# Optimization experiments

Hardware: AMD Instinct MI355X
Metric: run time of the kernel (lower is better)

Reference implementation:

```python
import jax, jax.numpy as jnp
import numpy as np

E = 16          # n_routed_experts
Z = 8           # zero_expert_num
K = 4           # moe_topk
H = 1024        # hidden_size
I = 768         # moe_intermediate_size
T = 2048        # tokens
SCALE = 2.5     # routed_scaling_factor


def setup_inputs() -> dict:
    key = jax.random.key(0)
    ks = jax.random.split(key, 6)
    return {
        "hidden_states": jax.random.normal(ks[0], (T, H), dtype=jnp.float32),
        "num_global_tokens": T,
        "max_num_tokens_per_gpu": T,
        "w_router": jax.random.normal(ks[1], (E + Z, H), dtype=jnp.float32) * 0.02,
        "correction_bias": jnp.zeros((E + Z,), dtype=jnp.float32),
        "wg": jax.random.normal(ks[2], (E, I, H), dtype=jnp.float32) * 0.02,
        "wu": jax.random.normal(ks[3], (E, I, H), dtype=jnp.float32) * 0.02,
        "wd": jax.random.normal(ks[4], (E, H, I), dtype=jnp.float32) * 0.02,
    }


def reference(hidden_states, num_global_tokens, max_num_tokens_per_gpu,
              w_router, correction_bias, wg, wu, wd):
    x = hidden_states
    # ---- router gemm (always fp32) ----
    logits = x.astype(jnp.float32) @ w_router.T                      # [T, E+Z]
    # ---- DeepSeekV3-style top-k: sigmoid scores, bias only for selection ----
    scores = jax.nn.sigmoid(logits)
    _, topk_ids = jax.lax.top_k(scores + correction_bias[None, :], K)  # [T, K]
    w = jnp.take_along_axis(scores, topk_ids, axis=-1)               # [T, K]
    w = w / jnp.sum(w, axis=-1, keepdims=True)                       # renormalize
    w = w * SCALE                                                    # routed_scaling_factor
    # ---- zero-expert masking (identity type) ----
    zero_mask = topk_ids >= E                                        # [T, K]
    zero_w = jnp.sum(jnp.where(zero_mask, w, 0.0), axis=-1, keepdims=True)
    ids = jnp.where(zero_mask, 0, topk_ids)
    w = jnp.where(zero_mask, 0.0, w)
    # ---- combine weights per (token, expert); masked slots add 0.0 ----
    cw = jnp.zeros((x.shape[0], E), dtype=jnp.float32)
    cw = cw.at[jnp.arange(x.shape[0])[:, None], ids].add(w)          # [T, E]
    # ---- grouped silu-gated expert MLPs (dense compute + masked combine) ----
    g = jnp.einsum('th,eih->eti', x, wg)                             # [E, T, I]
    u = jnp.einsum('th,eih->eti', x, wu)
    a = jax.nn.silu(g) * u
    y = jnp.einsum('eti,ehi->eth', a, wd)                            # [E, T, H]
    routed = jnp.einsum('eth,te->th', y, cw)                         # [T, H]
    return routed + x * zero_w.astype(x.dtype)
```

## Files before the change

kernel.cpp:

```cpp
#include <hip/hip_runtime.h>
#include <hip/hip_bf16.h>
#include <math.h>

typedef __bf16 bf16x8 __attribute__((ext_vector_type(8)));
typedef float f32x4 __attribute__((ext_vector_type(4)));

#define T_TOK 2048
#define HD 1024
#define ID 768
#define NE 16
#define NEZ 24
#define NK 4
#define SCALE_F 2.5f

#define MFMA(a, b, c) __builtin_amdgcn_mfma_f32_16x16x32_bf16(a, b, c, 0, 0, 0)

__device__ __forceinline__ unsigned short f2bf(float f) {
  unsigned int u = __builtin_bit_cast(unsigned int, f);
  u += 0x7FFFu + ((u >> 16) & 1u);
  return (unsigned short)(u >> 16);
}

__device__ __forceinline__ bf16x8 cvt8(float4 a, float4 b) {
  bf16x8 t;
  t[0] = (__bf16)a.x; t[1] = (__bf16)a.y; t[2] = (__bf16)a.z; t[3] = (__bf16)a.w;
  t[4] = (__bf16)b.x; t[5] = (__bf16)b.y; t[6] = (__bf16)b.z; t[7] = (__bf16)b.w;
  return t;
}

__device__ __forceinline__ void gload16(const void* g, void* l) {
  __builtin_amdgcn_global_load_lds(
      (const __attribute__((address_space(1))) void*)(unsigned long long)(uintptr_t)g,
      (__attribute__((address_space(3))) void*)(uintptr_t)l, 16, 0, 0);
}

__global__ __launch_bounds__(256) void router_k(
    const float* __restrict__ x, const float* __restrict__ wr,
    const float* __restrict__ bias,
    int* __restrict__ counts, int* __restrict__ lists, float* __restrict__ wlist,
    unsigned short* __restrict__ xb, float* __restrict__ out) {
  const int wave = threadIdx.x >> 6, l = threadIdx.x & 63;
  const int t = blockIdx.x * 4 + wave;

  float4 xr[4];
#pragma unroll
  for (int c = 0; c < 4; ++c)
    xr[c] = *(const float4*)(x + (size_t)t * HD + c * 256 + l * 4);
#pragma unroll
  for (int c = 0; c < 4; ++c) {
    ushort4 h;
    h.x = f2bf(xr[c].x); h.y = f2bf(xr[c].y); h.z = f2bf(xr[c].z); h.w = f2bf(xr[c].w);
    *(ushort4*)(xb + (size_t)t * HD + c * 256 + l * 4) = h;
  }

  float acc[NEZ];
#pragma unroll 4
  for (int e = 0; e < NEZ; ++e) {
    float4 s = {0.f, 0.f, 0.f, 0.f};
#pragma unroll
    for (int c = 0; c < 4; ++c) {
      float4 w4 = *(const float4*)(wr + (size_t)e * HD + c * 256 + l * 4);
      s.x = fmaf(w4.x, xr[c].x, s.x); s.y = fmaf(w4.y, xr[c].y, s.y);
      s.z = fmaf(w4.z, xr[c].z, s.z); s.w = fmaf(w4.w, xr[c].w, s.w);
    }
    acc[e] = (s.x + s.y) + (s.z + s.w);
  }
#pragma unroll
  for (int s = 1; s < 64; s <<= 1) {
#pragma unroll
    for (int e = 0; e < NEZ; ++e) acc[e] += __shfl_xor(acc[e], s);
  }
  float sc[NEZ], scb[NEZ];
#pragma unroll
  for (int e = 0; e < NEZ; ++e) {
    float s = 1.f / (1.f + expf(-acc[e]));
    sc[e] = s;
    scb[e] = s + bias[e];
  }
  unsigned picked = 0;
  int ids[NK]; float wv[NK]; float ssum = 0.f;
#pragma unroll
  for (int k = 0; k < NK; ++k) {
    int best = 0; float bv = -1e30f; float bsc = 0.f;
#pragma unroll
    for (int e = 0; e < NEZ; ++e) {
      bool take = (((picked >> e) & 1u) == 0) && (scb[e] > bv);
      best = take ? e : best;
      bv = take ? scb[e] : bv;
      bsc = take ? sc[e] : bsc;
    }
    picked |= 1u << best;
    ids[k] = best; wv[k] = bsc; ssum += bsc;
  }
  const float inv = SCALE_F / ssum;
  float zw = 0.f;
#pragma unroll
  for (int k = 0; k < NK; ++k)
    zw += (ids[k] >= NE) ? wv[k] * inv : 0.f;
  if (l < NK) {
    int id = ids[l];
    if (id < NE) {
      int p = atomicAdd(&counts[id], 1);
      lists[id * T_TOK + p] = t;
      wlist[id * T_TOK + p] = wv[l] * inv;
    }
  }
#pragma unroll
  for (int c = 0; c < 4; ++c) {
    float4 o;
    o.x = xr[c].x * zw; o.y = xr[c].y * zw;
    o.z = xr[c].z * zw; o.w = xr[c].w * zw;
    *(float4*)(out + (size_t)t * HD + c * 256 + l * 4) = o;
  }
}

__global__ void scan_k(const int* __restrict__ counts, int* __restrict__ offs) {
  if (threadIdx.x == 0 && blockIdx.x == 0) {
    int s = 0;
    for (int e = 0; e < NE; ++e) { offs[e] = s; s += counts[e]; }
    offs[NE] = s;
  }
}

__global__ __launch_bounds__(256, 3) void gu_k(
    const unsigned short* __restrict__ xb,
    const float* __restrict__ wg, const float* __restrict__ wu,
    const int* __restrict__ counts, const int* __restrict__ offs,
    const int* __restrict__ lists, unsigned short* __restrict__ abuf) {
  const int b = blockIdx.x;
  const int L = (b & 7) * 384 + (b >> 3);
  const int e = L / 192;
  const int rem = L % 192;
  const int xs = rem / 16, ys = rem % 16;
  const int cnt = counts[e];
  const int m0 = ys * 128;
  if (m0 >= cnt) return;
  const int n0 = xs * 64;

  __shared__ int toks[128];
  __shared__ char lds[2][24576];

  const int tid = threadIdx.x;
  if (tid < 128) {
    int m = m0 + tid;
    toks[tid] = (m < cnt) ? lists[e * T_TOK + m] : 0;
  }
  __syncthreads();

  const unsigned short* asrc[2];
#pragma unroll
  for (int j = 0; j < 2; ++j) {
    int row = j * 64 + (tid >> 2);
    int c = ((tid & 3) - (row >> 1)) & 3;
    asrc[j] = xb + (size_t)toks[row] * HD + c * 8;
  }
  const size_t wbase = (size_t)e * ID * HD;
  const float* gsrc[2]; const float* usrc[2];
#pragma unroll
  for (int j = 0; j < 2; ++j) {
    int row = j * 32 + (tid >> 3);
    int c = ((tid & 7) - row) & 7;
    size_t ro = wbase + (size_t)(n0 + row) * HD + c * 4;
    gsrc[j] = wg + ro; usrc[j] = wu + ro;
  }

  const int wid = tid >> 6, l = tid & 63;
  const int wm = (wid >> 1) * 64, wn = (wid & 1) * 32;
  const int q = l >> 4, r = l & 15;

  f32x4 ag[4][2] = {}; f32x4 au[4][2] = {};

  auto stage = [&](int bb, int k0) {
    char* dst = &lds[bb][0] + tid * 16;
#pragma unroll
    for (int j = 0; j < 2; ++j) {
      gload16(asrc[j] + k0, dst + j * 4096);
      gload16(gsrc[j] + k0, dst + 8192 + j * 4096);
      gload16(usrc[j] + k0, dst + 16384 + j * 4096);
    }
  };
  auto comp = [&](int bb) {
    const char* base = &lds[bb][0];
    bf16x8 a[4];
#pragma unroll
    for (int fm = 0; fm < 4; ++fm) {
      int rr = wm + fm * 16 + r;
      int p = (q + (rr >> 1)) & 3;
      a[fm] = *(const bf16x8*)(base + rr * 64 + p * 16);
    }
#pragma unroll
    for (int fn = 0; fn < 2; ++fn) {
      int cc = wn + fn * 16 + r;
      int p0 = (2 * q + cc) & 7, p1 = (2 * q + 1 + cc) & 7;
      const char* pg = base + 8192 + cc * 128;
      const char* pu = base + 16384 + cc * 128;
      float4 g0 = *(const float4*)(pg + p0 * 16);
      float4 g1 = *(const float4*)(pg + p1 * 16);
      float4 u0 = *(const float4*)(pu + p0 * 16);
      float4 u1 = *(const float4*)(pu + p1 * 16);
      bf16x8 bg = cvt8(g0, g1), bu = cvt8(u0, u1);
#pragma unroll
      for (int fm = 0; fm < 4; ++fm) {
        ag[fm][fn] = MFMA(a[fm], bg, ag[fm][fn]);
        au[fm][fn] = MFMA(a[fm], bu, au[fm][fn]);
      }
    }
  };

  stage(0, 0);
  __syncthreads();
  for (int t = 0; t < 32; t += 2) {
    stage(1, (t + 1) * 32);
    comp(0);
    __syncthreads();
    if (t + 2 < 32) stage(0, (t + 2) * 32);
    comp(1);
    __syncthreads();
  }

  const int rowbase = offs[e] + m0;
#pragma unroll
  for (int fm = 0; fm < 4; ++fm)
#pragma unroll
    for (int fn = 0; fn < 2; ++fn)
#pragma unroll
      for (int i2 = 0; i2 < 4; ++i2) {
        int mr = wm + fm * 16 + q * 4 + i2;
        if (m0 + mr < cnt) {
          float g = ag[fm][fn][i2], u = au[fm][fn][i2];
          float s = 1.0f / (1.0f + expf(-g));
          float aa = g * s * u;
          int col = n0 + wn + fn * 16 + r;
          abuf[(size_t)(rowbase + mr) * ID + col] = f2bf(aa);
        }
      }
}

__global__ __launch_bounds__(256, 3) void dn_k(
    const unsigned short* __restrict__ abuf,
    const float* __restrict__ wd,
    const int* __restrict__ counts, const int* __restrict__ offs,
    const int* __restrict__ lists, const float* __restrict__ wlist,
    float* __restrict__ out) {
  const int b = blockIdx.x;
  const int L = (b & 7) * 256 + (b >> 3);
  const int e = L / 128;
  const int rem = L % 128;
  const int xs = rem / 16, ys = rem % 16;
  const int cnt = counts[e];
  const int m0 = ys * 128;
  if (m0 >= cnt) return;
  const int n0 = xs * 128;

  __shared__ int toks[128];
  __shared__ float wts[128];
  __shared__ char lds[2][24576];

  const int tid = threadIdx.x;
  if (tid < 128) {
    int m = m0 + tid;
    if (m < cnt) { toks[tid] = lists[e * T_TOK + m]; wts[tid] = wlist[e * T_TOK + m]; }
    else         { toks[tid] = 0;                    wts[tid] = 0.f; }
  }
  __syncthreads();

  const int rowbase = offs[e] + m0;
  const unsigned short* asrc[2];
#pragma unroll
  for (int j = 0; j < 2; ++j) {
    int row = j * 64 + (tid >> 2);
    int c = ((tid & 3) - (row >> 1)) & 3;
    int grow = (m0 + row < cnt) ? rowbase + row : rowbase;
    asrc[j] = abuf + (size_t)grow * ID + c * 8;
  }
  const float* bsrc[4];
#pragma unroll
  for (int j = 0; j < 4; ++j) {
    int row = j * 32 + (tid >> 3);
    int c = ((tid & 7) - row) & 7;
    bsrc[j] = wd + (size_t)e * HD * ID + (size_t)(n0 + row) * ID + c * 4;
  }

  const int wid = tid >> 6, l = tid & 63;
  const int wm = (wid >> 1) * 64, wn = (wid & 1) * 64;
  const int q = l >> 4, r = l & 15;

  f32x4 acc[4][4] = {};

  auto stage = [&](int bb, int k0) {
    char* dst = &lds[bb][0] + tid * 16;
#pragma unroll
    for (int j = 0; j < 2; ++j) gload16(asrc[j] + k0, dst + j * 4096);
#pragma unroll
    for (int j = 0; j < 4; ++j) gload16(bsrc[j] + k0, dst + 8192 + j * 4096);
  };
  auto comp = [&](int bb) {
    const char* base = &lds[bb][0];
    bf16x8 a[4];
#pragma unroll
    for (int fm = 0; fm < 4; ++fm) {
      int rr = wm + fm * 16 + r;
      int p = (q + (rr >> 1)) & 3;
      a[fm] = *(const bf16x8*)(base + rr * 64 + p * 16);
    }
#pragma unroll
    for (int fn = 0; fn < 4; ++fn) {
      int cc = wn + fn * 16 + r;
      int p0 = (2 * q + cc) & 7, p1 = (2 * q + 1 + cc) & 7;
      const char* pb = base + 8192 + cc * 128;
      float4 b0 = *(const float4*)(pb + p0 * 16);
      float4 b1 = *(const float4*)(pb + p1 * 16);
      bf16x8 bb2 = cvt8(b0, b1);
#pragma unroll
      for (int fm = 0; fm < 4; ++fm)
        acc[fm][fn] = MFMA(a[fm], bb2, acc[fm][fn]);
    }
  };

  stage(0, 0);
  __syncthreads();
  for (int t = 0; t < 24; t += 2) {
    stage(1, (t + 1) * 32);
    comp(0);
    __syncthreads();
    if (t + 2 < 24) stage(0, (t + 2) * 32);
    comp(1);
    __syncthreads();
  }

#pragma unroll
  for (int fm = 0; fm < 4; ++fm)
#pragma unroll
    for (int fn = 0; fn < 4; ++fn)
#pragma unroll
      for (int i2 = 0; i2 < 4; ++i2) {
        int mr = wm + fm * 16 + q * 4 + i2;
        if (m0 + mr < cnt) {
          int col = n0 + wn + fn * 16 + r;
          atomicAdd(&out[(size_t)toks[mr] * HD + col], acc[fm][fn][i2] * wts[mr]);
        }
      }
}

extern "C" void kernel_launch(void* const* d_in, const int* in_sizes, int n_in,
                              void* d_out, int out_size, void* d_ws, size_t ws_size,
                              hipStream_t stream) {
  (void)in_sizes; (void)n_in; (void)out_size; (void)ws_size;
  const float* x    = (const float*)d_in[0];
  const float* wr   = (const float*)d_in[3];
  const float* bias = (const float*)d_in[4];
  const float* wg   = (const float*)d_in[5];
  const float* wu   = (const float*)d_in[6];
  const float* wd   = (const float*)d_in[7];
  float* out = (float*)d_out;

  char* p = (char*)d_ws;
  auto alloc = [&](size_t bytes) {
    char* r = p;
    p += (bytes + 255) & ~(size_t)255;
    return r;
  };
  int*   counts  = (int*)alloc(NE * 4);
  int*   offs    = (int*)alloc((NE + 1) * 4);
  int*   lists   = (int*)alloc((size_t)NE * T_TOK * 4);
  float* wlist   = (float*)alloc((size_t)NE * T_TOK * 4);
  unsigned short* xb   = (unsigned short*)alloc((size_t)T_TOK * HD * 2);
  unsigned short* abuf = (unsigned short*)alloc((size_t)(T_TOK * NK + 128) * ID * 2);

  hipMemsetAsync(counts, 0, NE * 4, stream);
  router_k<<<T_TOK / 4, 256, 0, stream>>>(x, wr, bias, counts, lists, wlist, xb, out);
  scan_k<<<1, 64, 0, stream>>>(counts, offs);
  gu_k<<<3072, 256, 0, stream>>>(xb, wg, wu, counts, offs, lists, abuf);
  dn_k<<<2048, 256, 0, stream>>>(abuf, wd, counts, offs, lists, wlist, out);
}
```

Measured before the change: 128.7 us.

## Drop scan kernel, compute expert offsets inline, halve down-proj N tile

Removes the single-thread scan kernel launch and has each block of the gate/up and down kernels sum the preceding expert counts itself. The down-projection kernel now uses 128x64 tiles instead of 128x128, with half the LDS and accumulators, launch bounds raised to 4 blocks per SM, and twice as many blocks. Token ids and weights are read from global memory in the epilogue instead of being staged in shared memory. The aim is to cut launch overhead and raise occupancy and parallelism in the down GEMM, at the cost of reloading each A tile twice as often and doing more redundant offset work.

```diff
diff --git a/kernel.cpp b/kernel.cpp
--- a/kernel.cpp
+++ b/kernel.cpp
@@ -114,18 +114,10 @@
   }
 }
 
-__global__ void scan_k(const int* __restrict__ counts, int* __restrict__ offs) {
-  if (threadIdx.x == 0 && blockIdx.x == 0) {
-    int s = 0;
-    for (int e = 0; e < NE; ++e) { offs[e] = s; s += counts[e]; }
-    offs[NE] = s;
-  }
-}
-
 __global__ __launch_bounds__(256, 3) void gu_k(
     const unsigned short* __restrict__ xb,
     const float* __restrict__ wg, const float* __restrict__ wu,
-    const int* __restrict__ counts, const int* __restrict__ offs,
+    const int* __restrict__ counts,
     const int* __restrict__ lists, unsigned short* __restrict__ abuf) {
   const int b = blockIdx.x;
   const int L = (b & 7) * 384 + (b >> 3);
@@ -137,6 +129,9 @@
   if (m0 >= cnt) return;
   const int n0 = xs * 64;
 
+  int offs_e = 0;
+  for (int i = 0; i < e; ++i) offs_e += counts[i];
+
   __shared__ int toks[128];
   __shared__ char lds[2][24576];
 
@@ -218,7 +213,7 @@
     __syncthreads();
   }
 
-  const int rowbase = offs[e] + m0;
+  const int rowbase = offs_e + m0;
 #pragma unroll
   for (int fm = 0; fm < 4; ++fm)
 #pragma unroll
@@ -236,63 +231,59 @@
       }
 }
 
-__global__ __launch_bounds__(256, 3) void dn_k(
+__global__ __launch_bounds__(256, 4) void dn_k(
     const unsigned short* __restrict__ abuf,
     const float* __restrict__ wd,
-    const int* __restrict__ counts, const int* __restrict__ offs,
+    const int* __restrict__ counts,
     const int* __restrict__ lists, const float* __restrict__ wlist,
     float* __restrict__ out) {
   const int b = blockIdx.x;
-  const int L = (b & 7) * 256 + (b >> 3);
-  const int e = L / 128;
-  const int rem = L % 128;
+  const int L = (b & 7) * 512 + (b >> 3);
+  const int e = L / 256;
+  const int rem = L % 256;
   const int xs = rem / 16, ys = rem % 16;
   const int cnt = counts[e];
   const int m0 = ys * 128;
   if (m0 >= cnt) return;
-  const int n0 = xs * 128;
-
-  __shared__ int toks[128];
-  __shared__ float wts[128];
-  __shared__ char lds[2][24576];
+  const int n0 = xs * 64;
+
+  int offs_e = 0;
+  for (int i = 0; i < e; ++i) offs_e += counts[i];
+
+  __shared__ char lds[2][16384];
 
   const int tid = threadIdx.x;
-  if (tid < 128) {
-    int m = m0 + tid;
-    if (m < cnt) { toks[tid] = lists[e * T_TOK + m]; wts[tid] = wlist[e * T_TOK + m]; }
-    else         { toks[tid] = 0;                    wts[tid] = 0.f; }
-  }
-  __syncthreads();
-
-  const int rowbase = offs[e] + m0;
+
   const unsigned short* asrc[2];
 #pragma unroll
   for (int j = 0; j < 2; ++j) {
     int row = j * 64 + (tid >> 2);
     int c = ((tid & 3) - (row >> 1)) & 3;
-    int grow = (m0 + row < cnt) ? rowbase + row : rowbase;
-    asrc[j] = abuf + (size_t)grow * ID + c * 8;
-  }
-  const float* bsrc[4];
-#pragma unroll
-  for (int j = 0; j < 4; ++j) {
-    int row = j * 32 + (tid >> 3);
-    int c = ((tid & 7) - row) & 7;
+    int m = m0 + row; if (m >= cnt) m = cnt - 1;
+    asrc[j] = abuf + (size_t)(offs_e + m) * ID + c * 8;
+  }
+  const float* bsrc[2];
+#pragma unroll
+  for (int j = 0; j < 2; ++j) {
+    int u = j * 256 + tid;
+    int row = u >> 3;
+    int c = ((u & 7) - row) & 7;
     bsrc[j] = wd + (size_t)e * HD * ID + (size_t)(n0 + row) * ID + c * 4;
   }
 
   const int wid = tid >> 6, l = tid & 63;
-  const int wm = (wid >> 1) * 64, wn = (wid & 1) * 64;
+  const int wm = (wid >> 1) * 64, wn = (wid & 1) * 32;
   const int q = l >> 4, r = l & 15;
 
-  f32x4 acc[4][4] = {};
+  f32x4 acc[4][2] = {};
 
   auto stage = [&](int bb, int k0) {
     char* dst = &lds[bb][0] + tid * 16;
 #pragma unroll
-    for (int j = 0; j < 2; ++j) gload16(asrc[j] + k0, dst + j * 4096);
-#pragma unroll
-    for (int j = 0; j < 4; ++j) gload16(bsrc[j] + k0, dst + 8192 + j * 4096);
+    for (int j = 0; j < 2; ++j) {
+      gload16(asrc[j] + k0, dst + j * 4096);
+      gload16(bsrc[j] + k0, dst + 8192 + j * 4096);
+    }
   };
   auto comp = [&](int bb) {
     const char* base = &lds[bb][0];
@@ -304,7 +295,7 @@
       a[fm] = *(const bf16x8*)(base + rr * 64 + p * 16);
     }
 #pragma unroll
-    for (int fn = 0; fn < 4; ++fn) {
+    for (int fn = 0; fn < 2; ++fn) {
       int cc = wn + fn * 16 + r;
       int p0 = (2 * q + cc) & 7, p1 = (2 * q + 1 + cc) & 7;
       const char* pb = base + 8192 + cc * 128;
@@ -329,17 +320,21 @@
   }
 
 #pragma unroll
-  for (int fm = 0; fm < 4; ++fm)
-#pragma unroll
-    for (int fn = 0; fn < 4; ++fn)
-#pragma unroll
-      for (int i2 = 0; i2 < 4; ++i2) {
-        int mr = wm + fm * 16 + q * 4 + i2;
-        if (m0 + mr < cnt) {
+  for (int fm = 0; fm < 4; ++fm) {
+#pragma unroll
+    for (int i2 = 0; i2 < 4; ++i2) {
+      int mr = wm + fm * 16 + q * 4 + i2;
+      if (m0 + mr < cnt) {
+        int tok = lists[e * T_TOK + m0 + mr];
+        float wt = wlist[e * T_TOK + m0 + mr];
+#pragma unroll
+        for (int fn = 0; fn < 2; ++fn) {
           int col = n0 + wn + fn * 16 + r;
-          atomicAdd(&out[(size_t)toks[mr] * HD + col], acc[fm][fn][i2] * wts[mr]);
+          atomicAdd(&out[(size_t)tok * HD + col], acc[fm][fn][i2] * wt);
         }
       }
+    }
+  }
 }
 
 extern "C" void kernel_launch(void* const* d_in, const int* in_sizes, int n_in,
@@ -361,7 +356,6 @@
     return r;
   };
   int*   counts  = (int*)alloc(NE * 4);
-  int*   offs    = (int*)alloc((NE + 1) * 4);
   int*   lists   = (int*)alloc((size_t)NE * T_TOK * 4);
   float* wlist   = (float*)alloc((size_t)NE * T_TOK * 4);
   unsigned short* xb   = (unsigned short*)alloc((size_t)T_TOK * HD * 2);
@@ -369,7 +363,6 @@
 
   hipMemsetAsync(counts, 0, NE * 4, stream);
   router_k<<<T_TOK / 4, 256, 0, stream>>>(x, wr, bias, counts, lists, wlist, xb, out);
-  scan_k<<<1, 64, 0, stream>>>(counts, offs);
-  gu_k<<<3072, 256, 0, stream>>>(xb, wg, wu, counts, offs, lists, abuf);
-  dn_k<<<2048, 256, 0, stream>>>(abuf, wd, counts, offs, lists, wlist, out);
-}
+  gu_k<<<3072, 256, 0, stream>>>(xb, wg, wu, counts, lists, abuf);
+  dn_k<<<4096, 256, 0, stream>>>(abuf, wd, counts, lists, wlist, out);
+}
```

Result: no change. 128.1 us, median of 2 (-0.4%).
